# Kernel optimization log

Hardware: AMD Instinct MI355X
Metric: run time of the kernel (lower is better)

The kernel has to match this reference:

```python
import jax, jax.numpy as jnp
import numpy as np

N_POI = 100000   # number of POIs
N_EDGE = 50000   # directed hyperedges
N_USER = 50000   # user hyperedges (multi-view)
NNZ = 1_000_000  # nonzeros per incidence matrix
D = 128          # embedding dim
L = 3            # num_layers


def spmm(rows, cols, vals, x, num_rows):
    """COO sparse @ dense: y[r] += vals * x[c]."""
    return jax.ops.segment_sum(vals[:, None] * x[cols], rows, num_segments=num_rows)


def hyper_net(pois, rows1, cols1, vals1, n1, rows2, cols2, vals2, n2, attn):
    """Chained two-hop sparse propagation with relu + residual, layer-attention fusion.
    Dropout omitted (eval mode / deterministic reference)."""
    embs = [pois]
    x = pois
    for _ in range(L):
        m = spmm(rows1, cols1, vals1, x, n1)      # [n1, D] aggregate to hyperedges/users
        m = spmm(rows2, cols2, vals2, m, n2)      # [N_POI, D] propagate back to POIs
        x = jax.nn.relu(m) + embs[-1]             # relu + residual
        embs.append(x)
    w = jax.nn.softmax(attn)                      # [L+1]
    return jnp.einsum('l,lnd->nd', w, jnp.stack(embs))


def setup_inputs() -> dict:
    key = jax.random.key(0)
    ks = jax.random.split(key, 16)
    inp = {
        'pois_embs': jax.random.normal(ks[0], (N_POI, D), dtype=jnp.float32),
        'tar_rows': jax.random.randint(ks[1], (NNZ,), 0, N_EDGE, dtype=jnp.int32),
        'tar_cols': jax.random.randint(ks[2], (NNZ,), 0, N_POI, dtype=jnp.int32),
        'tar_vals': jax.random.uniform(ks[3], (NNZ,), dtype=jnp.float32),
        'src_rows': jax.random.randint(ks[4], (NNZ,), 0, N_POI, dtype=jnp.int32),
        'src_cols': jax.random.randint(ks[5], (NNZ,), 0, N_EDGE, dtype=jnp.int32),
        'src_vals': jax.random.uniform(ks[6], (NNZ,), dtype=jnp.float32),
        'up_rows': jax.random.randint(ks[7], (NNZ,), 0, N_USER, dtype=jnp.int32),
        'up_cols': jax.random.randint(ks[8], (NNZ,), 0, N_POI, dtype=jnp.int32),
        'up_vals': jax.random.uniform(ks[9], (NNZ,), dtype=jnp.float32),
        'pu_rows': jax.random.randint(ks[10], (NNZ,), 0, N_POI, dtype=jnp.int32),
        'pu_cols': jax.random.randint(ks[11], (NNZ,), 0, N_USER, dtype=jnp.int32),
        'pu_vals': jax.random.uniform(ks[12], (NNZ,), dtype=jnp.float32),
        'attn_di': jnp.ones((L + 1,), dtype=jnp.float32),
        'attn_mv': jnp.ones((L + 1,), dtype=jnp.float32),
    }
    return inp


def reference(pois_embs, tar_rows, tar_cols, tar_vals, src_rows, src_cols, src_vals,
              up_rows, up_cols, up_vals, pu_rows, pu_cols, pu_vals, attn_di, attn_mv):
    # Directed hypergraph branch: msg_tar = HG_poi_tar @ x ; msg_src = HG_poi_src @ msg_tar
    di = hyper_net(pois_embs, tar_rows, tar_cols, tar_vals, N_EDGE,
                   src_rows, src_cols, src_vals, N_POI, attn_di)
    # Multi-view (user) hypergraph branch: HG_up @ x ; HG_pu @ msg
    mv = hyper_net(pois_embs, up_rows, up_cols, up_vals, N_USER,
                   pu_rows, pu_cols, pu_vals, N_POI, attn_mv)
    return di + mv
```

## Files before the change

kernel.cpp:

```cpp
#include <hip/hip_runtime.h>

#define NNZC   1000000
#define NPOI   100000
#define NEDGE  50000
#define NUSER  50000
#define DIM    128
#define NL     3

#define PB     64
#define NBKT   196
#define SCANN  (4 * NBKT * PB)

static inline int ceil_div(int a, int b) { return (a + b - 1) / b; }

typedef unsigned int uint32;

__device__ __forceinline__ float bfLO(uint32 u) { return __uint_as_float(u << 16); }
__device__ __forceinline__ float bfHI(uint32 u) { return __uint_as_float(u & 0xffff0000u); }
__device__ __forceinline__ uint32 bf16_rne(float f) {
    uint32 u = __float_as_uint(f);
    return (u + 0x7fffu + ((u >> 16) & 1u)) >> 16;
}
__device__ __forceinline__ uint32 bfPACK(float a, float b) {
    return bf16_rne(a) | (bf16_rne(b) << 16);
}
__device__ __forceinline__ uint32 csrPACK(int col, float val) {
    return ((uint32)col) | (bf16_rne(val) << 17);
}
__device__ __forceinline__ int   csrCOL(uint32 e) { return (int)(e & 0x1FFFFu); }
__device__ __forceinline__ float csrVAL(uint32 e) { return __uint_as_float((e >> 17) << 16); }

__device__ __constant__ const int c_nrows[4]  = { NEDGE, NPOI, NUSER, NPOI };
__device__ __constant__ const int c_cntoff[4] = { 0, NEDGE, NEDGE + NPOI, NEDGE + NPOI + NUSER };
__device__ __constant__ const int c_cap[4]    = { 64, 48, 64, 48 };
__device__ __constant__ const int c_shift[4]  = { 8, 9, 8, 9 };
__device__ __constant__ const long long c_elloff[4] = { 0, 3200000, 8000000, 11200000 };


__global__ __launch_bounds__(1024) void histH_kernel(
    const int* __restrict__ r0, const int* __restrict__ r1,
    const int* __restrict__ r2, const int* __restrict__ r3,
    int* __restrict__ histG) {
    __shared__ int h[NBKT];
    int m = blockIdx.y, p = blockIdx.x;
    for (int i = threadIdx.x; i < NBKT; i += 1024) h[i] = 0;
    __syncthreads();
    const int* r = (m == 0) ? r0 : (m == 1) ? r1 : (m == 2) ? r2 : r3;
    int shift = c_shift[m];
    int lo = p * (NNZC / PB), hi = lo + NNZC / PB;
    for (int i = lo + (int)threadIdx.x; i < hi; i += 1024)
        atomicAdd(&h[r[i] >> shift], 1);
    __syncthreads();
    for (int b = threadIdx.x; b < NBKT; b += 1024)
        histG[(m * NBKT + b) * PB + p] = h[b];
}

__global__ __launch_bounds__(256) void scan_kernel(int* __restrict__ g) {
    __shared__ int base[257];
    int t = threadIdx.x;
    const int chunk = SCANN / 256;
    int lo = t * chunk;
    int s = 0;
    for (int i = 0; i < chunk; i++) s += g[lo + i];
    base[t + 1] = s;
    __syncthreads();
    if (t == 0) {
        base[0] = 0;
        for (int i = 1; i <= 256; i++) base[i] += base[i - 1];
    }
    __syncthreads();
    int off = base[t];
    for (int i = 0; i < chunk; i++) { int v = g[lo + i]; g[lo + i] = off; off += v; }
    if (t == 255) g[SCANN] = base[256];
}

__global__ __launch_bounds__(1024) void scatS_kernel(
    const int* __restrict__ r0, const int* __restrict__ r1,
    const int* __restrict__ r2, const int* __restrict__ r3,
    const int* __restrict__ c0, const int* __restrict__ c1,
    const int* __restrict__ c2, const int* __restrict__ c3,
    const float* __restrict__ v0, const float* __restrict__ v1,
    const float* __restrict__ v2, const float* __restrict__ v3,
    const int* __restrict__ scanG, uint2* __restrict__ rec) {
    __shared__ int cur[NBKT];
    int m = blockIdx.y, p = blockIdx.x;
    for (int b = threadIdx.x; b < NBKT; b += 1024)
        cur[b] = scanG[(m * NBKT + b) * PB + p];
    __syncthreads();
    const int*   r = (m == 0) ? r0 : (m == 1) ? r1 : (m == 2) ? r2 : r3;
    const int*   c = (m == 0) ? c0 : (m == 1) ? c1 : (m == 2) ? c2 : c3;
    const float* v = (m == 0) ? v0 : (m == 1) ? v1 : (m == 2) ? v2 : v3;
    int shift = c_shift[m];
    int lo = p * (NNZC / PB), hi = lo + NNZC / PB;
    for (int i = lo + (int)threadIdx.x; i < hi; i += 1024) {
        int row = r[i];
        int pos = atomicAdd(&cur[row >> shift], 1);
        rec[pos] = make_uint2((uint32)row, csrPACK(c[i], v[i]));
    }
}

__global__ __launch_bounds__(512) void fillB_kernel(
    const int* __restrict__ scanG, const uint2* __restrict__ rec,
    int* __restrict__ counts_all, uint32* __restrict__ ell) {
    __shared__ int cnt[512];
    int bx = (int)blockIdx.x;
    int m = bx / NBKT, b = bx - m * NBKT;
    int shift = c_shift[m];
    int rowlo = b << shift;
    int bklen = 1 << shift;
    for (int i = threadIdx.x; i < bklen; i += 512) cnt[i] = 0;
    __syncthreads();
    int lo = scanG[(m * NBKT + b) * PB];
    int hi = scanG[(m * NBKT + b + 1) * PB];
    int cap = c_cap[m];
    uint32* ebase = ell + c_elloff[m];
    for (int i = lo + (int)threadIdx.x; i < hi; i += 512) {
        uint2 e = rec[i];
        int row = (int)e.x;
        int pos = atomicAdd(&cnt[row - rowlo], 1);
        ebase[(size_t)row * cap + pos] = e.y;
    }
    __syncthreads();
    int nrows_b = c_nrows[m] - rowlo;
    if (nrows_b > bklen) nrows_b = bklen;
    int* counts = counts_all + c_cntoff[m];
    for (int i = threadIdx.x; i < nrows_b; i += 512)
        counts[rowlo + i] = cnt[i];
}

__global__ void softmax4_kernel(const float* __restrict__ adi,
                                const float* __restrict__ amv,
                                float* __restrict__ w) {
    if (blockIdx.x == 0 && threadIdx.x == 0) {
        for (int b = 0; b < 2; b++) {
            const float* a = b ? amv : adi;
            float m = a[0];
            for (int l = 1; l < 4; l++) m = fmaxf(m, a[l]);
            float e[4]; float s = 0.f;
            for (int l = 0; l < 4; l++) { e[l] = __expf(a[l] - m); s += e[l]; }
            for (int l = 0; l < 4; l++) w[b * 4 + l] = e[l] / s;
        }
    }
}

__global__ void cast_bf16_kernel(const float* __restrict__ src, uint32* __restrict__ dst, int npairs) {
    int i = blockIdx.x * blockDim.x + threadIdx.x;
    if (i < npairs) {
        float2 f = *(const float2*)(src + (size_t)i * 2);
        dst[i] = bfPACK(f.x, f.y);
    }
}

#define GFMA(EV, UV) do { float _v = csrVAL(EV); \
    acc.x = fmaf(_v, bfLO(UV), acc.x); acc.y = fmaf(_v, bfHI(UV), acc.y); } while (0)

template<int CAP>
__global__ __launch_bounds__(256) void spmm1_kernel(
    const int* __restrict__ counts, const uint32* __restrict__ ell,
    const uint32* __restrict__ xbf, uint32* __restrict__ ybf, int n_rows) {
    int row = (blockIdx.x * blockDim.x + threadIdx.x) >> 6;
    int lane = threadIdx.x & 63;
    if (row >= n_rows) return;
    int cnt = counts[row];
    uint32 e = ell[(size_t)row * CAP + lane];
    float2 acc = make_float2(0.f, 0.f);
    int j = 0;
    for (; j + 8 <= cnt; j += 8) {
        uint32 e0 = __shfl(e, j),     e1 = __shfl(e, j + 1);
        uint32 e2 = __shfl(e, j + 2), e3 = __shfl(e, j + 3);
        uint32 e4 = __shfl(e, j + 4), e5 = __shfl(e, j + 5);
        uint32 e6 = __shfl(e, j + 6), e7 = __shfl(e, j + 7);
        uint32 u0 = xbf[(size_t)csrCOL(e0) * 64 + lane];
        uint32 u1 = xbf[(size_t)csrCOL(e1) * 64 + lane];
        uint32 u2 = xbf[(size_t)csrCOL(e2) * 64 + lane];
        uint32 u3 = xbf[(size_t)csrCOL(e3) * 64 + lane];
        uint32 u4 = xbf[(size_t)csrCOL(e4) * 64 + lane];
        uint32 u5 = xbf[(size_t)csrCOL(e5) * 64 + lane];
        uint32 u6 = xbf[(size_t)csrCOL(e6) * 64 + lane];
        uint32 u7 = xbf[(size_t)csrCOL(e7) * 64 + lane];
        GFMA(e0, u0); GFMA(e1, u1); GFMA(e2, u2); GFMA(e3, u3);
        GFMA(e4, u4); GFMA(e5, u5); GFMA(e6, u6); GFMA(e7, u7);
    }
    for (; j + 4 <= cnt; j += 4) {
        uint32 e0 = __shfl(e, j),     e1 = __shfl(e, j + 1);
        uint32 e2 = __shfl(e, j + 2), e3 = __shfl(e, j + 3);
        uint32 u0 = xbf[(size_t)csrCOL(e0) * 64 + lane];
        uint32 u1 = xbf[(size_t)csrCOL(e1) * 64 + lane];
        uint32 u2 = xbf[(size_t)csrCOL(e2) * 64 + lane];
        uint32 u3 = xbf[(size_t)csrCOL(e3) * 64 + lane];
        GFMA(e0, u0); GFMA(e1, u1); GFMA(e2, u2); GFMA(e3, u3);
    }
    for (; j < cnt; j++) {
        uint32 ej = __shfl(e, j);
        uint32 u = xbf[(size_t)csrCOL(ej) * 64 + lane];
        GFMA(ej, u);
    }
    ybf[(size_t)row * 64 + lane] = bfPACK(acc.x, acc.y);
}

template<int CAP>
__global__ __launch_bounds__(256) void spmm2_kernel(
    const int* __restrict__ counts, const uint32* __restrict__ ell,
    const uint32* __restrict__ mbf, const uint32* __restrict__ xinbf,
    uint32* __restrict__ xoutbf, int n_rows) {
    int row = (blockIdx.x * blockDim.x + threadIdx.x) >> 6;
    int lane = threadIdx.x & 63;
    if (row >= n_rows) return;
    int cnt = counts[row];
    uint32 e = ell[(size_t)row * CAP + lane];
    float2 acc = make_float2(0.f, 0.f);
    int j = 0;
    for (; j + 8 <= cnt; j += 8) {
        uint32 e0 = __shfl(e, j),     e1 = __shfl(e, j + 1);
        uint32 e2 = __shfl(e, j + 2), e3 = __shfl(e, j + 3);
        uint32 e4 = __shfl(e, j + 4), e5 = __shfl(e, j + 5);
        uint32 e6 = __shfl(e, j + 6), e7 = __shfl(e, j + 7);
        uint32 u0 = mbf[(size_t)csrCOL(e0) * 64 + lane];
        uint32 u1 = mbf[(size_t)csrCOL(e1) * 64 + lane];
        uint32 u2 = mbf[(size_t)csrCOL(e2) * 64 + lane];
        uint32 u3 = mbf[(size_t)csrCOL(e3) * 64 + lane];
        uint32 u4 = mbf[(size_t)csrCOL(e4) * 64 + lane];
        uint32 u5 = mbf[(size_t)csrCOL(e5) * 64 + lane];
        uint32 u6 = mbf[(size_t)csrCOL(e6) * 64 + lane];
        uint32 u7 = mbf[(size_t)csrCOL(e7) * 64 + lane];
        GFMA(e0, u0); GFMA(e1, u1); GFMA(e2, u2); GFMA(e3, u3);
        GFMA(e4, u4); GFMA(e5, u5); GFMA(e6, u6); GFMA(e7, u7);
    }
    for (; j + 4 <= cnt; j += 4) {
        uint32 e0 = __shfl(e, j),     e1 = __shfl(e, j + 1);
        uint32 e2 = __shfl(e, j + 2), e3 = __shfl(e, j + 3);
        uint32 u0 = mbf[(size_t)csrCOL(e0) * 64 + lane];
        uint32 u1 = mbf[(size_t)csrCOL(e1) * 64 + lane];
        uint32 u2 = mbf[(size_t)csrCOL(e2) * 64 + lane];
        uint32 u3 = mbf[(size_t)csrCOL(e3) * 64 + lane];
        GFMA(e0, u0); GFMA(e1, u1); GFMA(e2, u2); GFMA(e3, u3);
    }
    for (; j < cnt; j++) {
        uint32 ej = __shfl(e, j);
        uint32 u = mbf[(size_t)csrCOL(ej) * 64 + lane];
        GFMA(ej, u);
    }
    size_t o32 = (size_t)row * 64 + lane;
    uint32 ui = xinbf[o32];
    float xn0 = fmaxf(acc.x, 0.f) + bfLO(ui);
    float xn1 = fmaxf(acc.y, 0.f) + bfHI(ui);
    xoutbf[o32] = bfPACK(xn0, xn1);
}

__global__ void epi1_kernel(const float* __restrict__ pois,
                            const uint32* __restrict__ x1, const uint32* __restrict__ x2,
                            const uint32* __restrict__ x3, const float* __restrict__ w,
                            float* __restrict__ out) {
    int i = blockIdx.x * blockDim.x + threadIdx.x;
    if (i < NPOI * 64) {
        float w0 = w[0] + w[4];
        float2 pf = ((const float2*)pois)[i];
        uint32 u1 = x1[i], u2 = x2[i], u3 = x3[i];
        float o0 = w0 * pf.x + w[1] * bfLO(u1) + w[2] * bfLO(u2) + w[3] * bfLO(u3);
        float o1 = w0 * pf.y + w[1] * bfHI(u1) + w[2] * bfHI(u2) + w[3] * bfHI(u3);
        ((float2*)out)[i] = make_float2(o0, o1);
    }
}

__global__ void epi2_kernel(const uint32* __restrict__ x1, const uint32* __restrict__ x2,
                            const uint32* __restrict__ x3, const float* __restrict__ w,
                            float* __restrict__ out) {
    int i = blockIdx.x * blockDim.x + threadIdx.x;
    if (i < NPOI * 64) {
        uint32 u1 = x1[i], u2 = x2[i], u3 = x3[i];
        float2 ov = ((float2*)out)[i];
        ov.x += w[5] * bfLO(u1) + w[6] * bfLO(u2) + w[7] * bfLO(u3);
        ov.y += w[5] * bfHI(u1) + w[6] * bfHI(u2) + w[7] * bfHI(u3);
        ((float2*)out)[i] = ov;
    }
}

extern "C" void kernel_launch(void* const* d_in, const int* in_sizes, int n_in,
                              void* d_out, int out_size, void* d_ws, size_t ws_size,
                              hipStream_t stream) {
    const float* pois = (const float*)d_in[0];
    const int*   rows_in[4] = { (const int*)d_in[1], (const int*)d_in[4],
                                (const int*)d_in[7], (const int*)d_in[10] };
    const int*   cols_in[4] = { (const int*)d_in[2], (const int*)d_in[5],
                                (const int*)d_in[8], (const int*)d_in[11] };
    const float* vals_in[4] = { (const float*)d_in[3], (const float*)d_in[6],
                                (const float*)d_in[9], (const float*)d_in[12] };
    const float* attn_di = (const float*)d_in[13];
    const float* attn_mv = (const float*)d_in[14];
    float* out = (float*)d_out;

    const int NTOT = NEDGE + NPOI + NUSER + NPOI;
    const int cnt_off[4] = { 0, NEDGE, NEDGE + NPOI, NEDGE + NPOI + NUSER };
    const long long ell_off[4] = { 0, 3200000, 8000000, 11200000 };

    char* p = (char*)d_ws;
    float*  wsoft      = (float*)p;  p += 256;
    int*    counts_all = (int*)p;    p += (size_t)NTOT * 4;
    p = (char*)(((size_t)p + 255) & ~255ull);
    int*    scanG      = (int*)p;    p += (size_t)(SCANN + 64) * 4;
    p = (char*)(((size_t)p + 255) & ~255ull);
    uint32* ell        = (uint32*)p; p += (size_t)16000000 * 4;
    uint32* mbf        = (uint32*)p; p += (size_t)NEDGE * 64 * 4;
    uint32* poisbf     = (uint32*)p; p += (size_t)NPOI * 64 * 4;
    uint32* xl[3];
    for (int l = 0; l < 3; l++) { xl[l] = (uint32*)p; p += (size_t)NPOI * 64 * 4; }
    uint2* rec = (uint2*)xl[0];
    (void)ws_size; (void)out_size; (void)n_in; (void)in_sizes;

    histH_kernel<<<dim3(PB, 4), 1024, 0, stream>>>(
        rows_in[0], rows_in[1], rows_in[2], rows_in[3], scanG);
    scan_kernel<<<1, 256, 0, stream>>>(scanG);
    scatS_kernel<<<dim3(PB, 4), 1024, 0, stream>>>(
        rows_in[0], rows_in[1], rows_in[2], rows_in[3],
        cols_in[0], cols_in[1], cols_in[2], cols_in[3],
        vals_in[0], vals_in[1], vals_in[2], vals_in[3],
        scanG, rec);
    fillB_kernel<<<4 * NBKT, 512, 0, stream>>>(scanG, rec, counts_all, ell);

    softmax4_kernel<<<1, 64, 0, stream>>>(attn_di, attn_mv, wsoft);
    cast_bf16_kernel<<<ceil_div(NPOI * 64, 256), 256, 0, stream>>>(pois, poisbf, NPOI * 64);

    for (int br = 0; br < 2; br++) {
        int m1i = br ? 2 : 0;
        int m2i = br ? 3 : 1;
        const int* cn1 = counts_all + cnt_off[m1i];
        const int* cn2 = counts_all + cnt_off[m2i];
        const uint32* el1 = ell + ell_off[m1i];
        const uint32* el2 = ell + ell_off[m2i];
        const int n1 = 50000;
        const uint32* xcur = poisbf;
        for (int l = 1; l <= NL; l++) {
            spmm1_kernel<64><<<ceil_div(n1, 4), 256, 0, stream>>>(cn1, el1, xcur, mbf, n1);
            spmm2_kernel<48><<<ceil_div(NPOI, 4), 256, 0, stream>>>(
                cn2, el2, mbf, xcur, xl[l - 1], NPOI);
            xcur = xl[l - 1];
        }
        if (br == 0)
            epi1_kernel<<<ceil_div(NPOI * 64, 256), 256, 0, stream>>>(
                pois, xl[0], xl[1], xl[2], wsoft, out);
        else
            epi2_kernel<<<ceil_div(NPOI * 64, 256), 256, 0, stream>>>(
                xl[0], xl[1], xl[2], wsoft, out);
    }
}
```

Measured before the change: 781.8 us.

## Read ELL entries via wave-uniform vector loads instead of shuffles; double partition blocks

The SpMM kernels now make the row index and count wave-uniform with readfirstlane. They read ELL entries as uniform uint4 loads, which the compiler can turn into scalar loads, replacing the per-lane ELL load and the cross-lane shuffles. Index arithmetic moves from size_t to 32-bit ints to cut address computation. Separately, the histogram and scatter preprocessing uses 128 partition blocks instead of 64, with a rounded split of the range. The 32-bit indexing relies on the arrays staying small enough not to overflow, and the wider loads assume 16-byte-aligned ELL rows.

```diff
diff --git a/kernel.cpp b/kernel.cpp
--- a/kernel.cpp
+++ b/kernel.cpp
@@ -7,7 +7,7 @@
 #define DIM    128
 #define NL     3
 
-#define PB     64
+#define PB     128
 #define NBKT   196
 #define SCANN  (4 * NBKT * PB)
 
@@ -47,7 +47,8 @@
     __syncthreads();
     const int* r = (m == 0) ? r0 : (m == 1) ? r1 : (m == 2) ? r2 : r3;
     int shift = c_shift[m];
-    int lo = p * (NNZC / PB), hi = lo + NNZC / PB;
+    int lo = (int)(((long long)NNZC * p) >> 7);
+    int hi = (int)(((long long)NNZC * (p + 1)) >> 7);
     for (int i = lo + (int)threadIdx.x; i < hi; i += 1024)
         atomicAdd(&h[r[i] >> shift], 1);
     __syncthreads();
@@ -91,7 +92,8 @@
     const int*   c = (m == 0) ? c0 : (m == 1) ? c1 : (m == 2) ? c2 : c3;
     const float* v = (m == 0) ? v0 : (m == 1) ? v1 : (m == 2) ? v2 : v3;
     int shift = c_shift[m];
-    int lo = p * (NNZC / PB), hi = lo + NNZC / PB;
+    int lo = (int)(((long long)NNZC * p) >> 7);
+    int hi = (int)(((long long)NNZC * (p + 1)) >> 7);
     for (int i = lo + (int)threadIdx.x; i < hi; i += 1024) {
         int row = r[i];
         int pos = atomicAdd(&cur[row >> shift], 1);
@@ -151,51 +153,49 @@
     }
 }
 
-#define GFMA(EV, UV) do { float _v = csrVAL(EV); \
-    acc.x = fmaf(_v, bfLO(UV), acc.x); acc.y = fmaf(_v, bfHI(UV), acc.y); } while (0)
+#define GPROC(E, U) do { float _v = csrVAL(E); \
+    acc.x = fmaf(_v, bfLO(U), acc.x); acc.y = fmaf(_v, bfHI(U), acc.y); } while (0)
 
 template<int CAP>
 __global__ __launch_bounds__(256) void spmm1_kernel(
     const int* __restrict__ counts, const uint32* __restrict__ ell,
     const uint32* __restrict__ xbf, uint32* __restrict__ ybf, int n_rows) {
-    int row = (blockIdx.x * blockDim.x + threadIdx.x) >> 6;
-    int lane = threadIdx.x & 63;
+    int row = (int)((blockIdx.x * blockDim.x + threadIdx.x) >> 6);
+    int lane = (int)(threadIdx.x & 63);
     if (row >= n_rows) return;
-    int cnt = counts[row];
-    uint32 e = ell[(size_t)row * CAP + lane];
+    row = __builtin_amdgcn_readfirstlane(row);
+    int cnt = __builtin_amdgcn_readfirstlane(counts[row]);
+    const uint32* erow = ell + row * CAP;
+    const uint4*  erow4 = (const uint4*)erow;
     float2 acc = make_float2(0.f, 0.f);
     int j = 0;
     for (; j + 8 <= cnt; j += 8) {
-        uint32 e0 = __shfl(e, j),     e1 = __shfl(e, j + 1);
-        uint32 e2 = __shfl(e, j + 2), e3 = __shfl(e, j + 3);
-        uint32 e4 = __shfl(e, j + 4), e5 = __shfl(e, j + 5);
-        uint32 e6 = __shfl(e, j + 6), e7 = __shfl(e, j + 7);
-        uint32 u0 = xbf[(size_t)csrCOL(e0) * 64 + lane];
-        uint32 u1 = xbf[(size_t)csrCOL(e1) * 64 + lane];
-        uint32 u2 = xbf[(size_t)csrCOL(e2) * 64 + lane];
-        uint32 u3 = xbf[(size_t)csrCOL(e3) * 64 + lane];
-        uint32 u4 = xbf[(size_t)csrCOL(e4) * 64 + lane];
-        uint32 u5 = xbf[(size_t)csrCOL(e5) * 64 + lane];
-        uint32 u6 = xbf[(size_t)csrCOL(e6) * 64 + lane];
-        uint32 u7 = xbf[(size_t)csrCOL(e7) * 64 + lane];
-        GFMA(e0, u0); GFMA(e1, u1); GFMA(e2, u2); GFMA(e3, u3);
-        GFMA(e4, u4); GFMA(e5, u5); GFMA(e6, u6); GFMA(e7, u7);
+        uint4 qa = erow4[j >> 2], qb = erow4[(j >> 2) + 1];
+        uint32 u0 = xbf[csrCOL(qa.x) * 64 + lane];
+        uint32 u1 = xbf[csrCOL(qa.y) * 64 + lane];
+        uint32 u2 = xbf[csrCOL(qa.z) * 64 + lane];
+        uint32 u3 = xbf[csrCOL(qa.w) * 64 + lane];
+        uint32 u4 = xbf[csrCOL(qb.x) * 64 + lane];
+        uint32 u5 = xbf[csrCOL(qb.y) * 64 + lane];
+        uint32 u6 = xbf[csrCOL(qb.z) * 64 + lane];
+        uint32 u7 = xbf[csrCOL(qb.w) * 64 + lane];
+        GPROC(qa.x, u0); GPROC(qa.y, u1); GPROC(qa.z, u2); GPROC(qa.w, u3);
+        GPROC(qb.x, u4); GPROC(qb.y, u5); GPROC(qb.z, u6); GPROC(qb.w, u7);
     }
     for (; j + 4 <= cnt; j += 4) {
-        uint32 e0 = __shfl(e, j),     e1 = __shfl(e, j + 1);
-        uint32 e2 = __shfl(e, j + 2), e3 = __shfl(e, j + 3);
-        uint32 u0 = xbf[(size_t)csrCOL(e0) * 64 + lane];
-        uint32 u1 = xbf[(size_t)csrCOL(e1) * 64 + lane];
-        uint32 u2 = xbf[(size_t)csrCOL(e2) * 64 + lane];
-        uint32 u3 = xbf[(size_t)csrCOL(e3) * 64 + lane];
-        GFMA(e0, u0); GFMA(e1, u1); GFMA(e2, u2); GFMA(e3, u3);
+        uint4 q = erow4[j >> 2];
+        uint32 u0 = xbf[csrCOL(q.x) * 64 + lane];
+        uint32 u1 = xbf[csrCOL(q.y) * 64 + lane];
+        uint32 u2 = xbf[csrCOL(q.z) * 64 + lane];
+        uint32 u3 = xbf[csrCOL(q.w) * 64 + lane];
+        GPROC(q.x, u0); GPROC(q.y, u1); GPROC(q.z, u2); GPROC(q.w, u3);
     }
     for (; j < cnt; j++) {
-        uint32 ej = __shfl(e, j);
-        uint32 u = xbf[(size_t)csrCOL(ej) * 64 + lane];
-        GFMA(ej, u);
-    }
-    ybf[(size_t)row * 64 + lane] = bfPACK(acc.x, acc.y);
+        uint32 e = erow[j];
+        uint32 u = xbf[csrCOL(e) * 64 + lane];
+        GPROC(e, u);
+    }
+    ybf[row * 64 + lane] = bfPACK(acc.x, acc.y);
 }
 
 template<int CAP>
@@ -203,44 +203,42 @@
     const int* __restrict__ counts, const uint32* __restrict__ ell,
     const uint32* __restrict__ mbf, const uint32* __restrict__ xinbf,
     uint32* __restrict__ xoutbf, int n_rows) {
-    int row = (blockIdx.x * blockDim.x + threadIdx.x) >> 6;
-    int lane = threadIdx.x & 63;
+    int row = (int)((blockIdx.x * blockDim.x + threadIdx.x) >> 6);
+    int lane = (int)(threadIdx.x & 63);
     if (row >= n_rows) return;
-    int cnt = counts[row];
-    uint32 e = ell[(size_t)row * CAP + lane];
+    row = __builtin_amdgcn_readfirstlane(row);
+    int cnt = __builtin_amdgcn_readfirstlane(counts[row]);
+    const uint32* erow = ell + row * CAP;
+    const uint4*  erow4 = (const uint4*)erow;
     float2 acc = make_float2(0.f, 0.f);
     int j = 0;
     for (; j + 8 <= cnt; j += 8) {
-        uint32 e0 = __shfl(e, j),     e1 = __shfl(e, j + 1);
-        uint32 e2 = __shfl(e, j + 2), e3 = __shfl(e, j + 3);
-        uint32 e4 = __shfl(e, j + 4), e5 = __shfl(e, j + 5);
-        uint32 e6 = __shfl(e, j + 6), e7 = __shfl(e, j + 7);
-        uint32 u0 = mbf[(size_t)csrCOL(e0) * 64 + lane];
-        uint32 u1 = mbf[(size_t)csrCOL(e1) * 64 + lane];
-        uint32 u2 = mbf[(size_t)csrCOL(e2) * 64 + lane];
-        uint32 u3 = mbf[(size_t)csrCOL(e3) * 64 + lane];
-        uint32 u4 = mbf[(size_t)csrCOL(e4) * 64 + lane];
-        uint32 u5 = mbf[(size_t)csrCOL(e5) * 64 + lane];
-        uint32 u6 = mbf[(size_t)csrCOL(e6) * 64 + lane];
-        uint32 u7 = mbf[(size_t)csrCOL(e7) * 64 + lane];
-        GFMA(e0, u0); GFMA(e1, u1); GFMA(e2, u2); GFMA(e3, u3);
-        GFMA(e4, u4); GFMA(e5, u5); GFMA(e6, u6); GFMA(e7, u7);
+        uint4 qa = erow4[j >> 2], qb = erow4[(j >> 2) + 1];
+        uint32 u0 = mbf[csrCOL(qa.x) * 64 + lane];
+        uint32 u1 = mbf[csrCOL(qa.y) * 64 + lane];
+        uint32 u2 = mbf[csrCOL(qa.z) * 64 + lane];
+        uint32 u3 = mbf[csrCOL(qa.w) * 64 + lane];
+        uint32 u4 = mbf[csrCOL(qb.x) * 64 + lane];
+        uint32 u5 = mbf[csrCOL(qb.y) * 64 + lane];
+        uint32 u6 = mbf[csrCOL(qb.z) * 64 + lane];
+        uint32 u7 = mbf[csrCOL(qb.w) * 64 + lane];
+        GPROC(qa.x, u0); GPROC(qa.y, u1); GPROC(qa.z, u2); GPROC(qa.w, u3);
+        GPROC(qb.x, u4); GPROC(qb.y, u5); GPROC(qb.z, u6); GPROC(qb.w, u7);
     }
     for (; j + 4 <= cnt; j += 4) {
-        uint32 e0 = __shfl(e, j),     e1 = __shfl(e, j + 1);
-        uint32 e2 = __shfl(e, j + 2), e3 = __shfl(e, j + 3);
-        uint32 u0 = mbf[(size_t)csrCOL(e0) * 64 + lane];
-        uint32 u1 = mbf[(size_t)csrCOL(e1) * 64 + lane];
-        uint32 u2 = mbf[(size_t)csrCOL(e2) * 64 + lane];
-        uint32 u3 = mbf[(size_t)csrCOL(e3) * 64 + lane];
-        GFMA(e0, u0); GFMA(e1, u1); GFMA(e2, u2); GFMA(e3, u3);
+        uint4 q = erow4[j >> 2];
+        uint32 u0 = mbf[csrCOL(q.x) * 64 + lane];
+        uint32 u1 = mbf[csrCOL(q.y) * 64 + lane];
+        uint32 u2 = mbf[csrCOL(q.z) * 64 + lane];
+        uint32 u3 = mbf[csrCOL(q.w) * 64 + lane];
+        GPROC(q.x, u0); GPROC(q.y, u1); GPROC(q.z, u2); GPROC(q.w, u3);
     }
     for (; j < cnt; j++) {
-        uint32 ej = __shfl(e, j);
-        uint32 u = mbf[(size_t)csrCOL(ej) * 64 + lane];
-        GFMA(ej, u);
-    }
-    size_t o32 = (size_t)row * 64 + lane;
+        uint32 e = erow[j];
+        uint32 u = mbf[csrCOL(e) * 64 + lane];
+        GPROC(e, u);
+    }
+    int o32 = row * 64 + lane;
     uint32 ui = xinbf[o32];
     float xn0 = fmaxf(acc.x, 0.f) + bfLO(ui);
     float xn1 = fmaxf(acc.y, 0.f) + bfHI(ui);
```

New measurement: 790.9 us. About the same (+1.2%).
